# Optimization experiments

Hardware: AMD Instinct MI355X
Metric: run time of the kernel (lower is better)

## Reference

```python
import jax, jax.numpy as jnp
import numpy as np

NUM_NODES = 100000
EMB_DIM = 64
NUM_EDGES = 1280000
NUM_LAYERS = 3


def setup_inputs() -> dict:
    key = jax.random.key(0)
    k1, k2 = jax.random.split(key)
    edge_index = jax.random.randint(k1, (2, NUM_EDGES), 0, NUM_NODES, dtype=jnp.int32)
    emb = jax.random.normal(k2, (NUM_NODES, EMB_DIM), dtype=jnp.float32) * 0.01
    return {"edge_index": edge_index, "emb": emb}


def _lgconv_norm(edge_index):
    # PyG gcn_norm without self-loops: deg over destination nodes,
    # norm_e = deg[src]^-0.5 * deg[dst]^-0.5
    src, dst = edge_index[0], edge_index[1]
    deg = jax.ops.segment_sum(jnp.ones((edge_index.shape[1],), jnp.float32), dst,
                              num_segments=NUM_NODES)
    dinv = jnp.where(deg > 0, jax.lax.rsqrt(jnp.maximum(deg, 1.0)), 0.0)
    return src, dst, dinv[src] * dinv[dst]


def reference(edge_index, emb):
    src, dst, w = _lgconv_norm(edge_index)
    x = emb
    out = x
    for _ in range(NUM_LAYERS):
        # message: gather source embeddings, scale, scatter-add to destination
        x = jax.ops.segment_sum(x[src] * w[:, None], dst, num_segments=NUM_NODES)
        out = out + x
    return out / (NUM_LAYERS + 1)
```

## Files before the change

### kernel.cpp

```cpp
#include <hip/hip_runtime.h>

#define N_NODES 100000
#define EMB 64
#define N_EDGES 1280000
#define N_E4 (N_EDGES / 4)

#define NBUCK 196
#define BUCK_SHIFT 9
#define BUCK_NODES 512
#define NBA 313
#define HTOT (NBUCK * NBA)
#define NBH ((HTOT + 1023) / 1024)

typedef unsigned long long u64;
typedef _Float16 f16;
typedef __attribute__((ext_vector_type(2))) _Float16 f16x2;

__global__ void bucket_hist_kernel(const int* __restrict__ dst, int* __restrict__ hist) {
    __shared__ int lh[NBUCK];
    for (int i = threadIdx.x; i < NBUCK; i += 256) lh[i] = 0;
    __syncthreads();
#pragma unroll
    for (int k = 0; k < 4; ++k) {
        int q = blockIdx.x * 1024 + k * 256 + threadIdx.x;
        if (q < N_E4) {
            int4 d4 = ((const int4*)dst)[q];
            atomicAdd(&lh[d4.x >> BUCK_SHIFT], 1);
            atomicAdd(&lh[d4.y >> BUCK_SHIFT], 1);
            atomicAdd(&lh[d4.z >> BUCK_SHIFT], 1);
            atomicAdd(&lh[d4.w >> BUCK_SHIFT], 1);
        }
    }
    __syncthreads();
    for (int i = threadIdx.x; i < NBUCK; i += 256)
        hist[i * NBA + blockIdx.x] = lh[i];
}

__global__ void hist_scan1_kernel(int* __restrict__ hist, int* __restrict__ hbs) {
    __shared__ int lds[256];
    int base = blockIdx.x * 1024;
    int vals[4];
    int tsum = 0;
#pragma unroll
    for (int k = 0; k < 4; ++k) {
        int i = base + threadIdx.x * 4 + k;
        vals[k] = (i < HTOT) ? hist[i] : 0;
        tsum += vals[k];
    }
    lds[threadIdx.x] = tsum;
    __syncthreads();
    for (int off = 1; off < 256; off <<= 1) {
        int v = (threadIdx.x >= (unsigned)off) ? lds[threadIdx.x - off] : 0;
        __syncthreads();
        lds[threadIdx.x] += v;
        __syncthreads();
    }
    int run = lds[threadIdx.x] - tsum;
    if (threadIdx.x == 255) hbs[blockIdx.x] = lds[255];
    #pragma unroll
    for (int k = 0; k < 4; ++k) {
        int i = base + threadIdx.x * 4 + k;
        if (i < HTOT) hist[i] = run;
        run += vals[k];
    }
}

__global__ void hist_scan2_kernel(int* __restrict__ hbs) {
    __shared__ int lds[64];
    int v = (threadIdx.x < (unsigned)NBH) ? hbs[threadIdx.x] : 0;
    lds[threadIdx.x] = v;
    __syncthreads();
    for (int off = 1; off < 64; off <<= 1) {
        int t = (threadIdx.x >= (unsigned)off) ? lds[threadIdx.x - off] : 0;
        __syncthreads();
        lds[threadIdx.x] += t;
        __syncthreads();
    }
    if (threadIdx.x < (unsigned)NBH) hbs[threadIdx.x] = lds[threadIdx.x] - v;
}

__global__ void bucket_scatter_kernel(const int* __restrict__ src, const int* __restrict__ dst,
                                      const int* __restrict__ hist, const int* __restrict__ hbs,
                                      int* __restrict__ bedge) {
    __shared__ int cur[NBUCK];
    for (int i = threadIdx.x; i < NBUCK; i += 256) {
        int idx = i * NBA + blockIdx.x;
        cur[i] = hist[idx] + hbs[idx >> 10];
    }
    __syncthreads();
#pragma unroll
    for (int k = 0; k < 4; ++k) {
        int q = blockIdx.x * 1024 + k * 256 + threadIdx.x;
        if (q < N_E4) {
            int4 d4 = ((const int4*)dst)[q];
            int4 s4 = ((const int4*)src)[q];
            int p;
            p = atomicAdd(&cur[d4.x >> BUCK_SHIFT], 1);
            bedge[p] = s4.x | ((d4.x & (BUCK_NODES - 1)) << 17);
            p = atomicAdd(&cur[d4.y >> BUCK_SHIFT], 1);
            bedge[p] = s4.y | ((d4.y & (BUCK_NODES - 1)) << 17);
            p = atomicAdd(&cur[d4.z >> BUCK_SHIFT], 1);
            bedge[p] = s4.z | ((d4.z & (BUCK_NODES - 1)) << 17);
            p = atomicAdd(&cur[d4.w >> BUCK_SHIFT], 1);
            bedge[p] = s4.w | ((d4.w & (BUCK_NODES - 1)) << 17);
        }
    }
}

__global__ void bucket_build_kernel(const int* __restrict__ hist, const int* __restrict__ hbs,
                                    const int* __restrict__ bedge,
                                    int* __restrict__ col, int* __restrict__ row_start,
                                    float* __restrict__ dinv, float* __restrict__ rdinv) {
    __shared__ int lh[BUCK_NODES];
    __shared__ int sc[256];
    __shared__ int cur[BUCK_NODES];
    int k = blockIdx.x;
    int tid = threadIdx.x;
    int i0 = k * NBA;
    int beg = hist[i0] + hbs[i0 >> 10];
    int end;
    if (k + 1 < NBUCK) {
        int i1 = (k + 1) * NBA;
        end = hist[i1] + hbs[i1 >> 10];
    } else {
        end = N_EDGES;
    }
    lh[tid] = 0;
    lh[tid + 256] = 0;
    __syncthreads();
    for (int i = beg + tid; i < end; i += 256)
        atomicAdd(&lh[((unsigned)bedge[i]) >> 17], 1);
    __syncthreads();
    int v0 = lh[2 * tid];
    int v1 = lh[2 * tid + 1];
    int tsum = v0 + v1;
    sc[tid] = tsum;
    __syncthreads();
    for (int off = 1; off < 256; off <<= 1) {
        int v = (tid >= off) ? sc[tid - off] : 0;
        __syncthreads();
        sc[tid] += v;
        __syncthreads();
    }
    int texcl = sc[tid] - tsum;
    cur[2 * tid] = texcl;
    cur[2 * tid + 1] = texcl + v0;
    __syncthreads();
    for (int i = tid; i < BUCK_NODES; i += 256) {
        int node = k * BUCK_NODES + i;
        if (node <= N_NODES) {
            row_start[node] = beg + cur[i];
            if (node < N_NODES) {
                int d = lh[i];
                float fd = (float)d;
                dinv[node]  = (d > 0) ? rsqrtf(fd) : 0.0f;
                rdinv[node] = (d > 0) ? sqrtf(fd) : 0.0f;
            }
        }
    }
    for (int i = beg + tid; i < end; i += 256) {
        unsigned pe = (unsigned)bedge[i];
        int r = atomicAdd(&cur[pe >> 17], 1);
        col[beg + r] = (int)(pe & 0x1FFFFu);
    }
}

__global__ void y0_kernel(const float* __restrict__ emb, const float* __restrict__ dinv,
                          f16* __restrict__ y0) {
    int i = blockIdx.x * blockDim.x + threadIdx.x;
    const int n4 = N_NODES * EMB / 4;
    if (i < n4) {
        float dv = dinv[i >> 4];
        float4 v = ((const float4*)emb)[i];
        f16 h[4] = {(f16)(v.x * dv), (f16)(v.y * dv), (f16)(v.z * dv), (f16)(v.w * dv)};
        ((u64*)y0)[i] = *(const u64*)h;
    }
}

template <bool FINAL>
__global__ void gather_kernel(const int* __restrict__ row_start, const int* __restrict__ col,
                              const float* __restrict__ dinv, const float* __restrict__ rdinv,
                              const f16* __restrict__ yin, f16* __restrict__ yout,
                              const float* __restrict__ emb,
                              const f16* __restrict__ y1, const f16* __restrict__ y2,
                              float* __restrict__ out) {
    unsigned int gid = blockIdx.x * blockDim.x + threadIdx.x;
    unsigned int row = gid >> 6;
    int lane = (int)(gid & 63u);
    int s = lane >> 5;
    int j = lane & 31;
    if (row >= N_NODES) return;
    int beg = row_start[row];
    int end = row_start[row + 1];
    const f16* yj = yin + 2 * j;
    float accx = 0.0f, accy = 0.0f;
    for (int cb = beg; cb < end; cb += 64) {
        int idx = cb + lane;
        int ci = 0;
        if (idx < end) ci = col[idx];
        int n = end - cb;
        if (n > 64) n = 64;
        int kk = 0;
        for (; kk + 8 <= n; kk += 8) {
            int c0 = __shfl(ci, kk + s);
            int c1 = __shfl(ci, kk + s + 2);
            int c2 = __shfl(ci, kk + s + 4);
            int c3 = __shfl(ci, kk + s + 6);
            unsigned u0 = *(const unsigned*)(yj + (unsigned)c0 * EMB);
            unsigned u1 = *(const unsigned*)(yj + (unsigned)c1 * EMB);
            unsigned u2 = *(const unsigned*)(yj + (unsigned)c2 * EMB);
            unsigned u3 = *(const unsigned*)(yj + (unsigned)c3 * EMB);
            f16x2 h0 = __builtin_bit_cast(f16x2, u0);
            f16x2 h1 = __builtin_bit_cast(f16x2, u1);
            f16x2 h2 = __builtin_bit_cast(f16x2, u2);
            f16x2 h3 = __builtin_bit_cast(f16x2, u3);
            accx += (float)h0.x + (float)h1.x + (float)h2.x + (float)h3.x;
            accy += (float)h0.y + (float)h1.y + (float)h2.y + (float)h3.y;
        }
        if (kk + 4 <= n) {
            int c0 = __shfl(ci, kk + s);
            int c1 = __shfl(ci, kk + s + 2);
            unsigned u0 = *(const unsigned*)(yj + (unsigned)c0 * EMB);
            unsigned u1 = *(const unsigned*)(yj + (unsigned)c1 * EMB);
            f16x2 h0 = __builtin_bit_cast(f16x2, u0);
            f16x2 h1 = __builtin_bit_cast(f16x2, u1);
            accx += (float)h0.x + (float)h1.x;
            accy += (float)h0.y + (float)h1.y;
            kk += 4;
        }
        for (; kk < n; ++kk) {
            int c = __shfl(ci, kk);
            if (s == (kk & 1)) {
                unsigned u = *(const unsigned*)(yj + (unsigned)c * EMB);
                f16x2 h = __builtin_bit_cast(f16x2, u);
                accx += (float)h.x;
                accy += (float)h.y;
            }
        }
    }
    accx += __shfl_xor(accx, 32);
    accy += __shfl_xor(accy, 32);
    if (s == 0) {
        float dv = dinv[row];
        unsigned int o = row * EMB + 2 * (unsigned)j;
        if (!FINAL) {
            float sc = dv * dv;
            f16x2 h;
            h.x = (f16)(accx * sc);
            h.y = (f16)(accy * sc);
            *(unsigned*)(yout + o) = __builtin_bit_cast(unsigned, h);
        } else {
            float rv = rdinv[row];
            float2 e2 = *(const float2*)(emb + o);
            f16x2 a = __builtin_bit_cast(f16x2, *(const unsigned*)(y1 + o));
            f16x2 b = __builtin_bit_cast(f16x2, *(const unsigned*)(y2 + o));
            float rx = 0.25f * (e2.x + rv * ((float)a.x + (float)b.x) + dv * accx);
            float ry = 0.25f * (e2.y + rv * ((float)a.y + (float)b.y) + dv * accy);
            __builtin_nontemporal_store(rx, out + o);
            __builtin_nontemporal_store(ry, out + o + 1);
        }
    }
}

extern "C" void kernel_launch(void* const* d_in, const int* in_sizes, int n_in,
                              void* d_out, int out_size, void* d_ws, size_t ws_size,
                              hipStream_t stream) {
    const int*   edge = (const int*)d_in[0];
    const int*   src  = edge;
    const int*   dst  = edge + N_EDGES;
    const float* emb  = (const float*)d_in[1];
    float*       out  = (float*)d_out;

    char* ws = (char*)d_ws;
    size_t off = 0;
    int* row_start = (int*)(ws + off); off += 400016;
    int* hbs       = (int*)(ws + off); off += 256;
    float* dinv    = (float*)(ws + off); off += 400000;
    float* rdinv   = (float*)(ws + off); off += 400000;
    int* hist      = (int*)(ws + off); off += (size_t)HTOT * 4 + 16;
    int* col       = (int*)(ws + off); off += (size_t)N_EDGES * 4;
    f16* y0        = (f16*)(ws + off); off += (size_t)N_NODES * EMB * 2;
    f16* y1        = (f16*)(ws + off); off += (size_t)N_NODES * EMB * 2;
    f16* y2        = (f16*)(ws + off); off += (size_t)N_NODES * EMB * 2;

    int* bedge = (int*)y1;

    bucket_hist_kernel<<<NBA, 256, 0, stream>>>(dst, hist);
    hist_scan1_kernel<<<NBH, 256, 0, stream>>>(hist, hbs);
    hist_scan2_kernel<<<1, 64, 0, stream>>>(hbs);
    bucket_scatter_kernel<<<NBA, 256, 0, stream>>>(src, dst, hist, hbs, bedge);
    bucket_build_kernel<<<NBUCK, 256, 0, stream>>>(hist, hbs, bedge, col, row_start,
                                                   dinv, rdinv);
    y0_kernel<<<(N_NODES * EMB / 4 + 255) / 256, 256, 0, stream>>>(emb, dinv, y0);

    const unsigned int gthreads = (unsigned int)N_NODES * EMB;
    const int gblocks = (int)((gthreads + 255) / 256);
    gather_kernel<false><<<gblocks, 256, 0, stream>>>(row_start, col, dinv, rdinv,
                                                      y0, y1, emb, y1, y2, out);
    gather_kernel<false><<<gblocks, 256, 0, stream>>>(row_start, col, dinv, rdinv,
                                                      y1, y2, emb, y1, y2, out);
    gather_kernel<true><<<gblocks, 256, 0, stream>>>(row_start, col, dinv, rdinv,
                                                     y2, (f16*)0, emb, y1, y2, out);
}
```

Baseline: 259.7 us.

## Shrink CSR build buckets to 128 nodes and fuse y0 scaling into build kernel

Cuts the bucket size from 512 to 128 nodes, so there are four times as many buckets and more blocks in the CSR build kernel, and each block does a smaller per-bucket sort. The per-block histogram scan changes to one node per thread, and the second-level scan grows to 256 entries to match the larger histogram. The separate y0 kernel is removed: each build block now converts its own nodes' embeddings to dinv-scaled fp16, saving one launch and a reread of dinv. In exchange the histogram and scatter stages handle a larger bucket table, and half of each build block's threads sit idle during the per-node phases.

```diff
diff --git a/kernel.cpp b/kernel.cpp
--- a/kernel.cpp
+++ b/kernel.cpp
@@ -5,9 +5,9 @@
 #define N_EDGES 1280000
 #define N_E4 (N_EDGES / 4)
 
-#define NBUCK 196
-#define BUCK_SHIFT 9
-#define BUCK_NODES 512
+#define NBUCK 782
+#define BUCK_SHIFT 7
+#define BUCK_NODES 128
 #define NBA 313
 #define HTOT (NBUCK * NBA)
 #define NBH ((HTOT + 1023) / 1024)
@@ -66,11 +66,11 @@
 }
 
 __global__ void hist_scan2_kernel(int* __restrict__ hbs) {
-    __shared__ int lds[64];
+    __shared__ int lds[256];
     int v = (threadIdx.x < (unsigned)NBH) ? hbs[threadIdx.x] : 0;
     lds[threadIdx.x] = v;
     __syncthreads();
-    for (int off = 1; off < 64; off <<= 1) {
+    for (int off = 1; off < 256; off <<= 1) {
         int t = (threadIdx.x >= (unsigned)off) ? lds[threadIdx.x - off] : 0;
         __syncthreads();
         lds[threadIdx.x] += t;
@@ -108,9 +108,10 @@
 }
 
 __global__ void bucket_build_kernel(const int* __restrict__ hist, const int* __restrict__ hbs,
-                                    const int* __restrict__ bedge,
+                                    const int* __restrict__ bedge, const float* __restrict__ emb,
                                     int* __restrict__ col, int* __restrict__ row_start,
-                                    float* __restrict__ dinv, float* __restrict__ rdinv) {
+                                    float* __restrict__ dinv, float* __restrict__ rdinv,
+                                    f16* __restrict__ y0) {
     __shared__ int lh[BUCK_NODES];
     __shared__ int sc[256];
     __shared__ int cur[BUCK_NODES];
@@ -125,16 +126,13 @@
     } else {
         end = N_EDGES;
     }
-    lh[tid] = 0;
-    lh[tid + 256] = 0;
+    if (tid < BUCK_NODES) lh[tid] = 0;
     __syncthreads();
     for (int i = beg + tid; i < end; i += 256)
         atomicAdd(&lh[((unsigned)bedge[i]) >> 17], 1);
     __syncthreads();
-    int v0 = lh[2 * tid];
-    int v1 = lh[2 * tid + 1];
-    int tsum = v0 + v1;
-    sc[tid] = tsum;
+    int own = (tid < BUCK_NODES) ? lh[tid] : 0;
+    sc[tid] = own;
     __syncthreads();
     for (int off = 1; off < 256; off <<= 1) {
         int v = (tid >= off) ? sc[tid - off] : 0;
@@ -142,38 +140,39 @@
         sc[tid] += v;
         __syncthreads();
     }
-    int texcl = sc[tid] - tsum;
-    cur[2 * tid] = texcl;
-    cur[2 * tid + 1] = texcl + v0;
-    __syncthreads();
-    for (int i = tid; i < BUCK_NODES; i += 256) {
-        int node = k * BUCK_NODES + i;
+    if (tid < BUCK_NODES) cur[tid] = sc[tid] - own;
+    __syncthreads();
+    if (tid < BUCK_NODES) {
+        int node = k * BUCK_NODES + tid;
         if (node <= N_NODES) {
-            row_start[node] = beg + cur[i];
+            row_start[node] = beg + cur[tid];
             if (node < N_NODES) {
-                int d = lh[i];
+                int d = lh[tid];
                 float fd = (float)d;
                 dinv[node]  = (d > 0) ? rsqrtf(fd) : 0.0f;
                 rdinv[node] = (d > 0) ? sqrtf(fd) : 0.0f;
             }
         }
     }
+    __syncthreads();
     for (int i = beg + tid; i < end; i += 256) {
         unsigned pe = (unsigned)bedge[i];
         int r = atomicAdd(&cur[pe >> 17], 1);
         col[beg + r] = (int)(pe & 0x1FFFFu);
     }
-}
-
-__global__ void y0_kernel(const float* __restrict__ emb, const float* __restrict__ dinv,
-                          f16* __restrict__ y0) {
-    int i = blockIdx.x * blockDim.x + threadIdx.x;
-    const int n4 = N_NODES * EMB / 4;
-    if (i < n4) {
-        float dv = dinv[i >> 4];
-        float4 v = ((const float4*)emb)[i];
-        f16 h[4] = {(f16)(v.x * dv), (f16)(v.y * dv), (f16)(v.z * dv), (f16)(v.w * dv)};
-        ((u64*)y0)[i] = *(const u64*)h;
+    int nbase = k * BUCK_NODES;
+#pragma unroll
+    for (int it = 0; it < (BUCK_NODES * 16) / 256; ++it) {
+        int i = it * 256 + tid;
+        int node = nbase + (i >> 4);
+        if (node < N_NODES) {
+            float dd = (float)lh[i >> 4];
+            float dv = (dd > 0.0f) ? rsqrtf(dd) : 0.0f;
+            int quad = i & 15;
+            float4 v = ((const float4*)emb)[(size_t)node * 16 + quad];
+            f16 h[4] = {(f16)(v.x * dv), (f16)(v.y * dv), (f16)(v.z * dv), (f16)(v.w * dv)};
+            ((u64*)y0)[(size_t)node * 16 + quad] = *(const u64*)h;
+        }
     }
 }
 
@@ -274,7 +273,7 @@
     char* ws = (char*)d_ws;
     size_t off = 0;
     int* row_start = (int*)(ws + off); off += 400016;
-    int* hbs       = (int*)(ws + off); off += 256;
+    int* hbs       = (int*)(ws + off); off += 1024;
     float* dinv    = (float*)(ws + off); off += 400000;
     float* rdinv   = (float*)(ws + off); off += 400000;
     int* hist      = (int*)(ws + off); off += (size_t)HTOT * 4 + 16;
@@ -287,11 +286,10 @@
 
     bucket_hist_kernel<<<NBA, 256, 0, stream>>>(dst, hist);
     hist_scan1_kernel<<<NBH, 256, 0, stream>>>(hist, hbs);
-    hist_scan2_kernel<<<1, 64, 0, stream>>>(hbs);
+    hist_scan2_kernel<<<1, 256, 0, stream>>>(hbs);
     bucket_scatter_kernel<<<NBA, 256, 0, stream>>>(src, dst, hist, hbs, bedge);
-    bucket_build_kernel<<<NBUCK, 256, 0, stream>>>(hist, hbs, bedge, col, row_start,
-                                                   dinv, rdinv);
-    y0_kernel<<<(N_NODES * EMB / 4 + 255) / 256, 256, 0, stream>>>(emb, dinv, y0);
+    bucket_build_kernel<<<NBUCK, 256, 0, stream>>>(hist, hbs, bedge, emb, col,
+                                                   row_start, dinv, rdinv, y0);
 
     const unsigned int gthreads = (unsigned int)N_NODES * EMB;
     const int gblocks = (int)((gthreads + 255) / 256);
```

Result: no change. 259.2 us (median of 2 runs) (-0.2%).
